# Optimization experiments

Measured on AMD Instinct MI355X. Metric: run time of the kernel, lower is better.

The kernel has to match this reference:

```python
import itertools
import jax, jax.numpy as jnp
import numpy as np

NUM_GROUPS = 2  # num_squeeze_group
LN_EPS = 1e-6


def setup_inputs() -> dict:
    key = jax.random.key(0)
    ks = jax.random.split(key, 8)
    B, F, D = 1024, 32, 64
    P = F * (F - 1) // 2  # 496 pairs
    OUT = 512
    g = NUM_GROUPS
    red = max(1, F * g * 2 // 4)  # reduction_ratio = 4 -> 32
    emb_size = F * D
    return {
        "x": jax.random.normal(ks[0], (B, F, D), jnp.float32),
        "W1": jax.random.normal(ks[1], (F * 2 * g, red), jnp.float32) * (1.0 / np.sqrt(F * 2 * g)),
        "b1": jnp.zeros((red,), jnp.float32),
        "W2": jax.random.normal(ks[2], (red, emb_size), jnp.float32) * (1.0 / np.sqrt(red)),
        "b2": jnp.zeros((emb_size,), jnp.float32),
        "ln_scale": jnp.ones((emb_size,), jnp.float32),
        "ln_bias": jnp.zeros((emb_size,), jnp.float32),
        "Wp": jax.random.normal(ks[3], (P, D, D), jnp.float32) * (1.0 / np.sqrt(D)),
        "bp": jnp.zeros((P, D), jnp.float32),
        "Wo": jax.random.normal(ks[4], (P, OUT), jnp.float32) * (1.0 / np.sqrt(P)),
        "bo": jnp.zeros((OUT,), jnp.float32),
    }


def _pair_indices(F):
    pairs = np.array(list(itertools.combinations(range(F), 2)), dtype=np.int32)
    return pairs[:, 0], pairs[:, 1]


def reference(x, W1, b1, W2, b2, ln_scale, ln_bias, Wp, bp, Wo, bo):
    B, F, D = x.shape
    g = NUM_GROUPS

    # ---- SENet ----
    xg = x.reshape(B, F, g, D // g)
    # per-field [max(g), mean(g)], concatenated over fields -> [B, F*2g]
    z = jnp.concatenate([xg.max(axis=-1), xg.mean(axis=-1)], axis=-1).reshape(B, F * 2 * g)
    a1 = jax.nn.relu(z @ W1 + b1)            # [B, red]
    weights = a1 @ W2 + b2                   # [B, F*D]
    flat = x.reshape(B, F * D)
    senet = flat * weights + flat            # skip connection
    # layer norm over last axis
    mu = senet.mean(axis=-1, keepdims=True)
    var = senet.var(axis=-1, keepdims=True)
    senet = (senet - mu) * jax.lax.rsqrt(var + LN_EPS) * ln_scale + ln_bias

    # ---- BiLinear ('interaction', use_plus=True) ----
    i_idx, j_idx = _pair_indices(F)
    xi = x[:, i_idx, :]                      # [B, P, D]
    xj = x[:, j_idx, :]                      # [B, P, D]
    proj = jnp.einsum('bpd,pde->bpe', xi, Wp) + bp  # per-pair Dense(D->D)
    dots = jnp.sum(proj * xj, axis=-1)       # [B, P] batched dot (bi-linear+)
    bilinear = dots @ Wo + bo                # [B, OUT]

    return jnp.concatenate([senet, bilinear], axis=-1)
```

## Files before the change

kernel.cpp:

```cpp
#include <hip/hip_runtime.h>
#include <hip/hip_bf16.h>

#define F_FEAT 32
#define D_DIM 64
#define B_SZ 1024
#define EMB 2048
#define P_PAIRS 496
#define KPAD 512
#define OUT_N 512
#define OUT_STRIDE 2560
#define LN_EPS 1e-6f

typedef __attribute__((ext_vector_type(8))) short bf16x8;
typedef __attribute__((ext_vector_type(4))) float f32x4;

__device__ inline ushort f2bf(float f) {
    union { float f; unsigned u; } a; a.f = f;
    unsigned u = a.u;
    unsigned r = (u + 0x7FFFu + ((u >> 16) & 1u)) >> 16;
    return (ushort)r;
}
__device__ inline float bf2f(ushort u) {
    union { unsigned u; float f; } a; a.u = ((unsigned)u) << 16;
    return a.f;
}

__global__ __launch_bounds__(512) void k_front(
        const float* __restrict__ x, ushort* __restrict__ xb,
        const float* __restrict__ W1, const float* __restrict__ b1,
        const float* __restrict__ W2, const float* __restrict__ b2,
        const float* __restrict__ ln_s, const float* __restrict__ ln_b,
        const float* __restrict__ Wp, ushort* __restrict__ Wpt,
        const float* __restrict__ Wo, ushort* __restrict__ Wot,
        ushort* __restrict__ db, float* __restrict__ out) {
    __shared__ union {
        struct {
            float xs[4][EMB];
            float zs[4][128];
            float a1s[4][32];
            float red[2][4][8];
            float mlpred[2][128];
        } sn;
        float tile[64][65];
    } sm;
    int t = threadIdx.x;
    int blk = blockIdx.x;

    if (blk < 256) {
        int b0 = blk * 4;

        for (int r = 0; r < 4; ++r) {
            const float4* src = reinterpret_cast<const float4*>(x + (size_t)(b0 + r) * EMB);
            float4 v = src[t];
            reinterpret_cast<float4*>(&sm.sn.xs[r][0])[t] = v;
            ushort4 o;
            o.x = f2bf(v.x); o.y = f2bf(v.y); o.z = f2bf(v.z); o.w = f2bf(v.w);
            *reinterpret_cast<ushort4*>(xb + (size_t)(b0 + r) * EMB + t * 4) = o;
        }
        __syncthreads();

        {
            int g2 = t >> 1, sub = t & 1;
            int r = g2 >> 6, fg = g2 & 63, f = fg >> 1, gg = fg & 1;
            const float* base = &sm.sn.xs[r][f * 64 + gg * 32 + sub * 16];
            float mx = -INFINITY, smv = 0.f;
#pragma unroll
            for (int q = 0; q < 16; ++q) {
                float v = base[(q + t) & 15];
                mx = fmaxf(mx, v); smv += v;
            }
            float mx2 = __shfl_xor(mx, 1);
            float sm2 = __shfl_xor(smv, 1);
            mx = fmaxf(mx, mx2); smv += sm2;
            if (sub == 0) {
                sm.sn.zs[r][f * 4 + gg]     = mx;
                sm.sn.zs[r][f * 4 + 2 + gg] = smv * (1.f / 32.f);
            }
        }
        __syncthreads();

        if (t < 256) {
            int chunk = t >> 7, c = t & 127;
            int r = c >> 5, cc = c & 31;
            float acc = 0.f;
            int k0 = chunk * 64;
#pragma unroll
            for (int k = 0; k < 64; ++k) acc += sm.sn.zs[r][k0 + k] * W1[(k0 + k) * 32 + cc];
            sm.sn.mlpred[chunk][c] = acc;
        }
        __syncthreads();
        if (t < 128) {
            int r = t >> 5, cc = t & 31;
            sm.sn.a1s[r][cc] = fmaxf(sm.sn.mlpred[0][t] + sm.sn.mlpred[1][t] + b1[cc], 0.f);
        }
        __syncthreads();

        float acc[4][4];
#pragma unroll
        for (int r = 0; r < 4; ++r)
#pragma unroll
            for (int u = 0; u < 4; ++u) acc[r][u] = 0.f;

        for (int k = 0; k < 32; ++k) {
            float a0 = sm.sn.a1s[0][k], a1v = sm.sn.a1s[1][k];
            float a2 = sm.sn.a1s[2][k], a3 = sm.sn.a1s[3][k];
#pragma unroll
            for (int u = 0; u < 4; ++u) {
                float wv = W2[k * EMB + t + 512 * u];
                acc[0][u] += a0 * wv; acc[1][u] += a1v * wv;
                acc[2][u] += a2 * wv; acc[3][u] += a3 * wv;
            }
        }
        float ssum[4], ssq[4];
#pragma unroll
        for (int r = 0; r < 4; ++r) { ssum[r] = 0.f; ssq[r] = 0.f; }
#pragma unroll
        for (int r = 0; r < 4; ++r) {
#pragma unroll
            for (int u = 0; u < 4; ++u) {
                int e = t + 512 * u;
                float w = acc[r][u] + b2[e];
                float s = sm.sn.xs[r][e] * (w + 1.0f);
                sm.sn.xs[r][e] = s;
                ssum[r] += s; ssq[r] += s * s;
            }
        }
        int lane = t & 63, w = t >> 6;
#pragma unroll
        for (int r = 0; r < 4; ++r) {
            float a = ssum[r], q = ssq[r];
            for (int off = 32; off; off >>= 1) { a += __shfl_down(a, off); q += __shfl_down(q, off); }
            if (lane == 0) { sm.sn.red[0][r][w] = a; sm.sn.red[1][r][w] = q; }
        }
        __syncthreads();
        float mu[4], rs[4];
#pragma unroll
        for (int r = 0; r < 4; ++r) {
            float a = 0.f, q = 0.f;
#pragma unroll
            for (int i = 0; i < 8; ++i) { a += sm.sn.red[0][r][i]; q += sm.sn.red[1][r][i]; }
            mu[r] = a * (1.f / 2048.f);
            float var = q * (1.f / 2048.f) - mu[r] * mu[r];
            rs[r] = rsqrtf(var + LN_EPS);
        }
#pragma unroll
        for (int r = 0; r < 4; ++r) {
#pragma unroll
            for (int u = 0; u < 4; ++u) {
                int e = t + 512 * u;
                float s = sm.sn.xs[r][e];
                out[(size_t)(b0 + r) * OUT_STRIDE + e] = (s - mu[r]) * rs[r] * ln_s[e] + ln_b[e];
            }
        }
    } else if (blk < 752) {
        int p = blk - 256;
        const float* src = Wp + (size_t)p * 4096;
        ushort* dst = Wpt + (size_t)p * 4096;
#pragma unroll
        for (int it = 0; it < 2; ++it) {
            int d = it * 32 + (t >> 4);
            int e4 = (t & 15) * 4;
            float4 v = *reinterpret_cast<const float4*>(src + d * 64 + e4);
            sm.tile[d][e4] = v.x; sm.tile[d][e4 + 1] = v.y;
            sm.tile[d][e4 + 2] = v.z; sm.tile[d][e4 + 3] = v.w;
        }
        __syncthreads();
#pragma unroll
        for (int it = 0; it < 2; ++it) {
            int e = it * 32 + (t >> 4);
            int d4 = (t & 15) * 4;
            ushort4 o;
            o.x = f2bf(sm.tile[d4][e]);     o.y = f2bf(sm.tile[d4 + 1][e]);
            o.z = f2bf(sm.tile[d4 + 2][e]); o.w = f2bf(sm.tile[d4 + 3][e]);
            *reinterpret_cast<ushort4*>(dst + e * 64 + d4) = o;
        }
    } else if (blk < 816) {
        int bidx = blk - 752;
        int k0 = (bidx & 7) * 64;
        int n0 = (bidx >> 3) * 64;
#pragma unroll
        for (int it = 0; it < 2; ++it) {
            int kr = it * 32 + (t >> 4);
            int nc = (t & 15) * 4;
            int k = k0 + kr;
            float4 v = {0.f, 0.f, 0.f, 0.f};
            if (k < P_PAIRS) v = *reinterpret_cast<const float4*>(Wo + (size_t)k * OUT_N + n0 + nc);
            sm.tile[kr][nc] = v.x; sm.tile[kr][nc + 1] = v.y;
            sm.tile[kr][nc + 2] = v.z; sm.tile[kr][nc + 3] = v.w;
        }
        __syncthreads();
#pragma unroll
        for (int it = 0; it < 2; ++it) {
            int nr = it * 32 + (t >> 4);
            int kc = (t & 15) * 4;
            ushort4 o;
            o.x = f2bf(sm.tile[kc][nr]);     o.y = f2bf(sm.tile[kc + 1][nr]);
            o.z = f2bf(sm.tile[kc + 2][nr]); o.w = f2bf(sm.tile[kc + 3][nr]);
            *reinterpret_cast<ushort4*>(Wot + (size_t)(n0 + nr) * KPAD + k0 + kc) = o;
        }
    } else {
        int tid = (blk - 816) * 512 + t;
        if (tid < B_SZ) {
            bf16x8 z = {0, 0, 0, 0, 0, 0, 0, 0};
            ushort* dstp = db + (size_t)tid * KPAD + P_PAIRS;
            *reinterpret_cast<bf16x8*>(dstp) = z;
            *reinterpret_cast<bf16x8*>(dstp + 8) = z;
        }
    }
}

__global__ __launch_bounds__(256) void k_dots(
        const ushort* __restrict__ xb, const ushort* __restrict__ Wpt,
        const float* __restrict__ bp, ushort* __restrict__ db) {
    int p = blockIdx.x >> 2;
    int q = blockIdx.x & 3;
    int i = 0, rem = p;
    while (rem >= F_FEAT - 1 - i) { rem -= F_FEAT - 1 - i; ++i; }
    int j = i + 1 + rem;

    int wave = threadIdx.x >> 6, lane = threadIdx.x & 63;
    int row = lane & 15, kg = lane >> 4;

    bf16x8 wfr[4][2];
#pragma unroll
    for (int nt = 0; nt < 4; ++nt)
#pragma unroll
        for (int ks = 0; ks < 2; ++ks)
            wfr[nt][ks] = *reinterpret_cast<const bf16x8*>(
                Wpt + (size_t)p * 4096 + (nt * 16 + row) * 64 + ks * 32 + kg * 8);

    f32x4 bb[4];
#pragma unroll
    for (int nt = 0; nt < 4; ++nt)
        bb[nt] = *reinterpret_cast<const f32x4*>(bp + p * 64 + nt * 16 + kg * 4);

    const ushort* xi_base = xb + (size_t)row * EMB + i * 64 + kg * 8;
    const ushort* xj_base = xb + (size_t)row * EMB + j * 64 + kg * 4;

    bf16x8 xifr[2][2];
    ushort4 xjw[2][4];

    auto loadit = [&](int it, int buf) {
        size_t boff = (size_t)(q * 256 + (wave * 4 + it) * 16) * EMB;
#pragma unroll
        for (int ks = 0; ks < 2; ++ks)
            xifr[buf][ks] = *reinterpret_cast<const bf16x8*>(xi_base + boff + ks * 32);
#pragma unroll
        for (int nt = 0; nt < 4; ++nt)
            xjw[buf][nt] = *reinterpret_cast<const ushort4*>(xj_base + boff + nt * 16);
    };

    loadit(0, 0);
#pragma unroll
    for (int it = 0; it < 4; ++it) {
        int cur = it & 1;
        if (it < 3) loadit(it + 1, cur ^ 1);

        f32x4 acc[4];
#pragma unroll
        for (int nt = 0; nt < 4; ++nt) {
            acc[nt] = bb[nt];
            acc[nt] = __builtin_amdgcn_mfma_f32_16x16x32_bf16(wfr[nt][0], xifr[cur][0], acc[nt], 0, 0, 0);
            acc[nt] = __builtin_amdgcn_mfma_f32_16x16x32_bf16(wfr[nt][1], xifr[cur][1], acc[nt], 0, 0, 0);
        }

        float v = 0.f;
#pragma unroll
        for (int nt = 0; nt < 4; ++nt) {
            v += acc[nt][0] * bf2f(xjw[cur][nt].x);
            v += acc[nt][1] * bf2f(xjw[cur][nt].y);
            v += acc[nt][2] * bf2f(xjw[cur][nt].z);
            v += acc[nt][3] * bf2f(xjw[cur][nt].w);
        }
        v += __shfl_xor(v, 16);
        v += __shfl_xor(v, 32);
        if (lane < 16) {
            int b0 = q * 256 + (wave * 4 + it) * 16;
            db[(size_t)(b0 + lane) * KPAD + p] = f2bf(v);
        }
    }
}

__global__ __launch_bounds__(256) void k_bilin2(
        const ushort* __restrict__ db, const ushort* __restrict__ Wot,
        const float* __restrict__ bo, float* __restrict__ out) {
    int mt  = blockIdx.x >> 4;
    int nt0 = blockIdx.x & 15;
    int wave = threadIdx.x >> 6, lane = threadIdx.x & 63;
    int wm = wave & 1, wn = wave >> 1;
    int row = lane & 15, kg = lane >> 4;
    int m0 = mt * 32 + wm * 16;
    int n0 = nt0 * 32 + wn * 16;

    f32x4 acc0 = {0.f, 0.f, 0.f, 0.f};
    f32x4 acc1 = {0.f, 0.f, 0.f, 0.f};
    const ushort* arow = db  + (size_t)(m0 + row) * KPAD + kg * 8;
    const ushort* brow = Wot + (size_t)(n0 + row) * KPAD + kg * 8;
#pragma unroll
    for (int ks = 0; ks < 16; ks += 2) {
        bf16x8 a0 = *reinterpret_cast<const bf16x8*>(arow + ks * 32);
        bf16x8 b0 = *reinterpret_cast<const bf16x8*>(brow + ks * 32);
        bf16x8 a1 = *reinterpret_cast<const bf16x8*>(arow + (ks + 1) * 32);
        bf16x8 b1 = *reinterpret_cast<const bf16x8*>(brow + (ks + 1) * 32);
        acc0 = __builtin_amdgcn_mfma_f32_16x16x32_bf16(a0, b0, acc0, 0, 0, 0);
        acc1 = __builtin_amdgcn_mfma_f32_16x16x32_bf16(a1, b1, acc1, 0, 0, 0);
    }
    int col = row;
    float bov = bo[n0 + col];
#pragma unroll
    for (int r = 0; r < 4; ++r) {
        size_t orow = (size_t)(m0 + kg * 4 + r) * OUT_STRIDE + 2048 + n0;
        out[orow + col] = acc0[r] + acc1[r] + bov;
    }
}

extern "C" void kernel_launch(void* const* d_in, const int* in_sizes, int n_in,
                              void* d_out, int out_size, void* d_ws, size_t ws_size,
                              hipStream_t stream) {
    const float* x    = (const float*)d_in[0];
    const float* W1   = (const float*)d_in[1];
    const float* b1   = (const float*)d_in[2];
    const float* W2   = (const float*)d_in[3];
    const float* b2   = (const float*)d_in[4];
    const float* ln_s = (const float*)d_in[5];
    const float* ln_b = (const float*)d_in[6];
    const float* Wp   = (const float*)d_in[7];
    const float* bp   = (const float*)d_in[8];
    const float* Wo   = (const float*)d_in[9];
    const float* bo   = (const float*)d_in[10];
    float* out = (float*)d_out;

    ushort* xb   = (ushort*)d_ws;
    ushort* wpt  = (ushort*)((char*)d_ws + 4194304);
    ushort* db   = (ushort*)((char*)d_ws + 4194304 + 4063232);
    ushort* wot  = (ushort*)((char*)d_ws + 4194304 + 4063232 + 1048576);

    k_front<<<818, 512, 0, stream>>>(x, xb, W1, b1, W2, b2, ln_s, ln_b,
                                     Wp, wpt, Wo, wot, db, out);
    k_dots<<<P_PAIRS * 4, 256, 0, stream>>>(xb, wpt, bp, db);
    k_bilin2<<<512, 256, 0, stream>>>(db, wot, bo, out);
}
```

Before: 57.61 us.

## Restructure SENet front kernel to one row per 256-thread block in registers

The SENet/LayerNorm part of the front kernel now processes one batch row per 256-thread block instead of four rows per 512-thread block. Each thread keeps its 8 elements in registers rather than staging them in shared memory, and reductions are done with shuffles. This cuts shared memory use and raises block count and occupancy. The trade-off is that each block now reads W2 once per row instead of once per four rows, roughly quadrupling W2 traffic (mostly served from L2). The Wp/Wo transpose branches are adjusted to fit 256 threads.

```diff
diff --git a/kernel.cpp b/kernel.cpp
--- a/kernel.cpp
+++ b/kernel.cpp
@@ -25,7 +25,7 @@
     return a.f;
 }
 
-__global__ __launch_bounds__(512) void k_front(
+__global__ __launch_bounds__(256) void k_front(
         const float* __restrict__ x, ushort* __restrict__ xb,
         const float* __restrict__ W1, const float* __restrict__ b1,
         const float* __restrict__ W2, const float* __restrict__ b2,
@@ -34,131 +34,122 @@
         const float* __restrict__ Wo, ushort* __restrict__ Wot,
         ushort* __restrict__ db, float* __restrict__ out) {
     __shared__ union {
+        float tile[64][65];
         struct {
-            float xs[4][EMB];
-            float zs[4][128];
-            float a1s[4][32];
-            float red[2][4][8];
-            float mlpred[2][128];
+            float zs[128];
+            float a1s[32];
+            float mlpred[8][32];
+            float red[2][4];
         } sn;
-        float tile[64][65];
     } sm;
     int t = threadIdx.x;
     int blk = blockIdx.x;
 
-    if (blk < 256) {
-        int b0 = blk * 4;
-
-        for (int r = 0; r < 4; ++r) {
-            const float4* src = reinterpret_cast<const float4*>(x + (size_t)(b0 + r) * EMB);
-            float4 v = src[t];
-            reinterpret_cast<float4*>(&sm.sn.xs[r][0])[t] = v;
-            ushort4 o;
-            o.x = f2bf(v.x); o.y = f2bf(v.y); o.z = f2bf(v.z); o.w = f2bf(v.w);
-            *reinterpret_cast<ushort4*>(xb + (size_t)(b0 + r) * EMB + t * 4) = o;
-        }
-        __syncthreads();
+    if (blk < 1024) {
+        int b = blk;
+        int e0 = t * 8;
+        const float* xrow = x + (size_t)b * EMB + e0;
+        float4 v0 = *reinterpret_cast<const float4*>(xrow);
+        float4 v1 = *reinterpret_cast<const float4*>(xrow + 4);
+        float xr[8] = {v0.x, v0.y, v0.z, v0.w, v1.x, v1.y, v1.z, v1.w};
+
+        bf16x8 ob;
+#pragma unroll
+        for (int u = 0; u < 8; ++u) ob[u] = (short)f2bf(xr[u]);
+        *reinterpret_cast<bf16x8*>(xb + (size_t)b * EMB + e0) = ob;
 
         {
-            int g2 = t >> 1, sub = t & 1;
-            int r = g2 >> 6, fg = g2 & 63, f = fg >> 1, gg = fg & 1;
-            const float* base = &sm.sn.xs[r][f * 64 + gg * 32 + sub * 16];
-            float mx = -INFINITY, smv = 0.f;
-#pragma unroll
-            for (int q = 0; q < 16; ++q) {
-                float v = base[(q + t) & 15];
-                mx = fmaxf(mx, v); smv += v;
+            float mx = xr[0], sum = xr[0];
+#pragma unroll
+            for (int u = 1; u < 8; ++u) { mx = fmaxf(mx, xr[u]); sum += xr[u]; }
+            float m2 = __shfl_xor(mx, 1), s2 = __shfl_xor(sum, 1);
+            mx = fmaxf(mx, m2); sum += s2;
+            m2 = __shfl_xor(mx, 2); s2 = __shfl_xor(sum, 2);
+            mx = fmaxf(mx, m2); sum += s2;
+            if ((t & 3) == 0) {
+                int f = t >> 3, gg = (t >> 2) & 1;
+                sm.sn.zs[f * 4 + gg]     = mx;
+                sm.sn.zs[f * 4 + 2 + gg] = sum * (1.f / 32.f);
             }
-            float mx2 = __shfl_xor(mx, 1);
-            float sm2 = __shfl_xor(smv, 1);
-            mx = fmaxf(mx, mx2); smv += sm2;
-            if (sub == 0) {
-                sm.sn.zs[r][f * 4 + gg]     = mx;
-                sm.sn.zs[r][f * 4 + 2 + gg] = smv * (1.f / 32.f);
-            }
-        }
-        __syncthreads();
-
-        if (t < 256) {
-            int chunk = t >> 7, c = t & 127;
-            int r = c >> 5, cc = c & 31;
+        }
+        __syncthreads();
+
+        {
+            int c = t & 31, chunk = t >> 5;
+            int k0 = chunk * 16;
             float acc = 0.f;
-            int k0 = chunk * 64;
-#pragma unroll
-            for (int k = 0; k < 64; ++k) acc += sm.sn.zs[r][k0 + k] * W1[(k0 + k) * 32 + cc];
+#pragma unroll
+            for (int kk = 0; kk < 16; ++kk)
+                acc += sm.sn.zs[k0 + kk] * W1[(k0 + kk) * 32 + c];
             sm.sn.mlpred[chunk][c] = acc;
         }
         __syncthreads();
-        if (t < 128) {
-            int r = t >> 5, cc = t & 31;
-            sm.sn.a1s[r][cc] = fmaxf(sm.sn.mlpred[0][t] + sm.sn.mlpred[1][t] + b1[cc], 0.f);
-        }
-        __syncthreads();
-
-        float acc[4][4];
-#pragma unroll
-        for (int r = 0; r < 4; ++r)
-#pragma unroll
-            for (int u = 0; u < 4; ++u) acc[r][u] = 0.f;
-
+        if (t < 32) {
+            float acc = b1[t];
+#pragma unroll
+            for (int ch = 0; ch < 8; ++ch) acc += sm.sn.mlpred[ch][t];
+            sm.sn.a1s[t] = fmaxf(acc, 0.f);
+        }
+        __syncthreads();
+
+        float acc[8];
+#pragma unroll
+        for (int u = 0; u < 8; ++u) acc[u] = 0.f;
         for (int k = 0; k < 32; ++k) {
-            float a0 = sm.sn.a1s[0][k], a1v = sm.sn.a1s[1][k];
-            float a2 = sm.sn.a1s[2][k], a3 = sm.sn.a1s[3][k];
-#pragma unroll
-            for (int u = 0; u < 4; ++u) {
-                float wv = W2[k * EMB + t + 512 * u];
-                acc[0][u] += a0 * wv; acc[1][u] += a1v * wv;
-                acc[2][u] += a2 * wv; acc[3][u] += a3 * wv;
-            }
-        }
-        float ssum[4], ssq[4];
-#pragma unroll
-        for (int r = 0; r < 4; ++r) { ssum[r] = 0.f; ssq[r] = 0.f; }
-#pragma unroll
-        for (int r = 0; r < 4; ++r) {
-#pragma unroll
-            for (int u = 0; u < 4; ++u) {
-                int e = t + 512 * u;
-                float w = acc[r][u] + b2[e];
-                float s = sm.sn.xs[r][e] * (w + 1.0f);
-                sm.sn.xs[r][e] = s;
-                ssum[r] += s; ssq[r] += s * s;
-            }
-        }
-        int lane = t & 63, w = t >> 6;
-#pragma unroll
-        for (int r = 0; r < 4; ++r) {
-            float a = ssum[r], q = ssq[r];
-            for (int off = 32; off; off >>= 1) { a += __shfl_down(a, off); q += __shfl_down(q, off); }
-            if (lane == 0) { sm.sn.red[0][r][w] = a; sm.sn.red[1][r][w] = q; }
-        }
-        __syncthreads();
-        float mu[4], rs[4];
-#pragma unroll
-        for (int r = 0; r < 4; ++r) {
-            float a = 0.f, q = 0.f;
-#pragma unroll
-            for (int i = 0; i < 8; ++i) { a += sm.sn.red[0][r][i]; q += sm.sn.red[1][r][i]; }
-            mu[r] = a * (1.f / 2048.f);
-            float var = q * (1.f / 2048.f) - mu[r] * mu[r];
-            rs[r] = rsqrtf(var + LN_EPS);
-        }
-#pragma unroll
-        for (int r = 0; r < 4; ++r) {
-#pragma unroll
-            for (int u = 0; u < 4; ++u) {
-                int e = t + 512 * u;
-                float s = sm.sn.xs[r][e];
-                out[(size_t)(b0 + r) * OUT_STRIDE + e] = (s - mu[r]) * rs[r] * ln_s[e] + ln_b[e];
-            }
-        }
-    } else if (blk < 752) {
-        int p = blk - 256;
+            float a = sm.sn.a1s[k];
+            float4 w0 = *reinterpret_cast<const float4*>(W2 + (size_t)k * EMB + e0);
+            float4 w1 = *reinterpret_cast<const float4*>(W2 + (size_t)k * EMB + e0 + 4);
+            acc[0] += a * w0.x; acc[1] += a * w0.y; acc[2] += a * w0.z; acc[3] += a * w0.w;
+            acc[4] += a * w1.x; acc[5] += a * w1.y; acc[6] += a * w1.z; acc[7] += a * w1.w;
+        }
+        float4 b2v0 = *reinterpret_cast<const float4*>(b2 + e0);
+        float4 b2v1 = *reinterpret_cast<const float4*>(b2 + e0 + 4);
+        float b2a[8] = {b2v0.x, b2v0.y, b2v0.z, b2v0.w, b2v1.x, b2v1.y, b2v1.z, b2v1.w};
+
+        float ssum = 0.f, ssq = 0.f;
+#pragma unroll
+        for (int u = 0; u < 8; ++u) {
+            float s = xr[u] * (acc[u] + b2a[u] + 1.0f);
+            xr[u] = s;
+            ssum += s; ssq += s * s;
+        }
+        int lane = t & 63, wv = t >> 6;
+        for (int off = 32; off; off >>= 1) {
+            ssum += __shfl_down(ssum, off);
+            ssq  += __shfl_down(ssq, off);
+        }
+        if (lane == 0) { sm.sn.red[0][wv] = ssum; sm.sn.red[1][wv] = ssq; }
+        __syncthreads();
+        float a = 0.f, q = 0.f;
+#pragma unroll
+        for (int i = 0; i < 4; ++i) { a += sm.sn.red[0][i]; q += sm.sn.red[1][i]; }
+        float mu = a * (1.f / 2048.f);
+        float var = q * (1.f / 2048.f) - mu * mu;
+        float rs = rsqrtf(var + LN_EPS);
+
+        float4 lsv0 = *reinterpret_cast<const float4*>(ln_s + e0);
+        float4 lsv1 = *reinterpret_cast<const float4*>(ln_s + e0 + 4);
+        float4 lbv0 = *reinterpret_cast<const float4*>(ln_b + e0);
+        float4 lbv1 = *reinterpret_cast<const float4*>(ln_b + e0 + 4);
+        float* orow = out + (size_t)b * OUT_STRIDE + e0;
+        float4 o0, o1;
+        o0.x = (xr[0] - mu) * rs * lsv0.x + lbv0.x;
+        o0.y = (xr[1] - mu) * rs * lsv0.y + lbv0.y;
+        o0.z = (xr[2] - mu) * rs * lsv0.z + lbv0.z;
+        o0.w = (xr[3] - mu) * rs * lsv0.w + lbv0.w;
+        o1.x = (xr[4] - mu) * rs * lsv1.x + lbv1.x;
+        o1.y = (xr[5] - mu) * rs * lsv1.y + lbv1.y;
+        o1.z = (xr[6] - mu) * rs * lsv1.z + lbv1.z;
+        o1.w = (xr[7] - mu) * rs * lsv1.w + lbv1.w;
+        *reinterpret_cast<float4*>(orow)     = o0;
+        *reinterpret_cast<float4*>(orow + 4) = o1;
+    } else if (blk < 1520) {
+        int p = blk - 1024;
         const float* src = Wp + (size_t)p * 4096;
         ushort* dst = Wpt + (size_t)p * 4096;
 #pragma unroll
-        for (int it = 0; it < 2; ++it) {
-            int d = it * 32 + (t >> 4);
+        for (int it = 0; it < 4; ++it) {
+            int d = it * 16 + (t >> 4);
             int e4 = (t & 15) * 4;
             float4 v = *reinterpret_cast<const float4*>(src + d * 64 + e4);
             sm.tile[d][e4] = v.x; sm.tile[d][e4 + 1] = v.y;
@@ -166,21 +157,21 @@
         }
         __syncthreads();
 #pragma unroll
-        for (int it = 0; it < 2; ++it) {
-            int e = it * 32 + (t >> 4);
+        for (int it = 0; it < 4; ++it) {
+            int e = it * 16 + (t >> 4);
             int d4 = (t & 15) * 4;
             ushort4 o;
             o.x = f2bf(sm.tile[d4][e]);     o.y = f2bf(sm.tile[d4 + 1][e]);
             o.z = f2bf(sm.tile[d4 + 2][e]); o.w = f2bf(sm.tile[d4 + 3][e]);
             *reinterpret_cast<ushort4*>(dst + e * 64 + d4) = o;
         }
-    } else if (blk < 816) {
-        int bidx = blk - 752;
+    } else if (blk < 1584) {
+        int bidx = blk - 1520;
         int k0 = (bidx & 7) * 64;
         int n0 = (bidx >> 3) * 64;
 #pragma unroll
-        for (int it = 0; it < 2; ++it) {
-            int kr = it * 32 + (t >> 4);
+        for (int it = 0; it < 4; ++it) {
+            int kr = it * 16 + (t >> 4);
             int nc = (t & 15) * 4;
             int k = k0 + kr;
             float4 v = {0.f, 0.f, 0.f, 0.f};
@@ -190,8 +181,8 @@
         }
         __syncthreads();
 #pragma unroll
-        for (int it = 0; it < 2; ++it) {
-            int nr = it * 32 + (t >> 4);
+        for (int it = 0; it < 4; ++it) {
+            int nr = it * 16 + (t >> 4);
             int kc = (t & 15) * 4;
             ushort4 o;
             o.x = f2bf(sm.tile[kc][nr]);     o.y = f2bf(sm.tile[kc + 1][nr]);
@@ -199,7 +190,7 @@
             *reinterpret_cast<ushort4*>(Wot + (size_t)(n0 + nr) * KPAD + k0 + kc) = o;
         }
     } else {
-        int tid = (blk - 816) * 512 + t;
+        int tid = (blk - 1584) * 256 + t;
         if (tid < B_SZ) {
             bf16x8 z = {0, 0, 0, 0, 0, 0, 0, 0};
             ushort* dstp = db + (size_t)tid * KPAD + P_PAIRS;
@@ -335,8 +326,8 @@
     ushort* db   = (ushort*)((char*)d_ws + 4194304 + 4063232);
     ushort* wot  = (ushort*)((char*)d_ws + 4194304 + 4063232 + 1048576);
 
-    k_front<<<818, 512, 0, stream>>>(x, xb, W1, b1, W2, b2, ln_s, ln_b,
-                                     Wp, wpt, Wo, wot, db, out);
+    k_front<<<1592, 256, 0, stream>>>(x, xb, W1, b1, W2, b2, ln_s, ln_b,
+                                      Wp, wpt, Wo, wot, db, out);
     k_dots<<<P_PAIRS * 4, 256, 0, stream>>>(xb, wpt, bp, db);
     k_bilin2<<<512, 256, 0, stream>>>(db, wot, bo, out);
 }
```

After: 67.38 us, median of 4. 1.17x slower.
